# Kernel optimization log

Measured on AMD Instinct MI355X. Metric: run time of the kernel, lower is better.

The kernel has to match this reference:

```python
import jax, jax.numpy as jnp
import numpy as np

GAMMA = 0.5

def setup_inputs() -> dict:
    key = jax.random.key(0)
    k1, k2 = jax.random.split(key)
    x = jax.random.normal(k1, (4096, 256), dtype=jnp.float32)
    W = jax.random.normal(k2, (256, 512), dtype=jnp.float32)
    return {"x": x, "W": W}

def reference(x, W):
    # difference: (B, D, N) = (B, D, 1) - (D, N)
    diff = x[:, :, None] - W[None, :, :]
    sq_dist = jnp.sum(diff * diff, axis=1)          # (B, N)
    return jnp.exp(-GAMMA * sq_dist)                # (B, N)
```

## Files before the change

kernel.cpp:

```cpp
#include <hip/hip_runtime.h>


#define GAMMA 0.5f
#define B_  4096
#define D_  256
#define N_  512
#define BM  64
#define BN  64
#define LDT 264

typedef __attribute__((ext_vector_type(8))) short bf16x8;
typedef __attribute__((ext_vector_type(4))) float f32x4;
typedef __attribute__((ext_vector_type(4))) unsigned short u16x4;
typedef __attribute__((ext_vector_type(4))) float float4v;

__device__ __forceinline__ unsigned short f2bf(float f) {
    union { float f; unsigned int i; } u; u.f = f;
    return (unsigned short)(u.i >> 16);
}
__device__ __forceinline__ float bf2f(unsigned short h) {
    union { unsigned int i; float f; } u; u.i = ((unsigned int)h) << 16;
    return u.f;
}

__global__ __launch_bounds__(256, 4)
void rbf_kernel(const float* __restrict__ x, const float* __restrict__ W,
                float* __restrict__ out) {
    __shared__ unsigned short xs[BM][LDT];
    __shared__ float x2s[BM];

    const int tid = threadIdx.x;

    const int bid = blockIdx.x;
    const int wgid = (bid & 7) * 64 + (bid >> 3);
    const int bx = wgid & 7;
    const int by = wgid >> 3;

    {
        const float4v* xg = (const float4v*)(x + (size_t)by * BM * D_);
        #pragma unroll
        for (int t = 0; t < 16; ++t) {
            int i = tid + t * 256;
            int r = i >> 6, c4 = i & 63;
            float4v v = xg[i];
            u16x4 p = { f2bf(v.x), f2bf(v.y), f2bf(v.z), f2bf(v.w) };
            *(u16x4*)&xs[r][c4 * 4] = p;
        }
    }
    __syncthreads();

    {
        int row = tid >> 2, q = tid & 3;
        float s = 0.f;
        #pragma unroll
        for (int c = 0; c < 8; ++c) {
            bf16x8 v = *(const bf16x8*)&xs[row][q * 64 + c * 8];
            #pragma unroll
            for (int j = 0; j < 8; ++j) { float f = bf2f((unsigned short)v[j]); s += f * f; }
        }
        s += __shfl_xor(s, 1);
        s += __shfl_xor(s, 2);
        if (q == 0) x2s[row] = s;
    }
    __syncthreads();

    const int l = tid & 63, w = tid >> 6;
    const int wr = w >> 1, wc = w & 1;
    const int lr = l & 15, g = l >> 4;

    const float* Wg = W + bx * BN + wc * 32 + lr;
    float w2p0 = 0.f, w2p1 = 0.f;
    f32x4 accs[2][2] = {{{0,0,0,0},{0,0,0,0}},{{0,0,0,0},{0,0,0,0}}};

    #pragma unroll
    for (int kk = 0; kk < 8; ++kk) {
        const int k0 = kk * 32 + g * 8;
        const float* wp = Wg + (size_t)k0 * N_;
        float w0[8], w1[8];
        #pragma unroll
        for (int j = 0; j < 8; ++j) {
            w0[j] = wp[(size_t)j * N_];
            w1[j] = wp[(size_t)j * N_ + 16];
        }
        bf16x8 b0, b1;
        #pragma unroll
        for (int j = 0; j < 8; ++j) {
            b0[j] = (short)f2bf(w0[j]); b1[j] = (short)f2bf(w1[j]);
            w2p0 += w0[j] * w0[j];      w2p1 += w1[j] * w1[j];
        }
        bf16x8 a0 = *(const bf16x8*)&xs[wr * 32 + lr][k0];
        bf16x8 a1 = *(const bf16x8*)&xs[wr * 32 + 16 + lr][k0];
        accs[0][0] = __builtin_amdgcn_mfma_f32_16x16x32_bf16(a0, b0, accs[0][0], 0, 0, 0);
        accs[0][1] = __builtin_amdgcn_mfma_f32_16x16x32_bf16(a0, b1, accs[0][1], 0, 0, 0);
        accs[1][0] = __builtin_amdgcn_mfma_f32_16x16x32_bf16(a1, b0, accs[1][0], 0, 0, 0);
        accs[1][1] = __builtin_amdgcn_mfma_f32_16x16x32_bf16(a1, b1, accs[1][1], 0, 0, 0);
    }

    w2p0 += __shfl_xor(w2p0, 16); w2p0 += __shfl_xor(w2p0, 32);
    w2p1 += __shfl_xor(w2p1, 16); w2p1 += __shfl_xor(w2p1, 32);

    const float c2l = -(GAMMA) * 1.4426950408889634f;
    float* outp = out + (size_t)(by * BM) * N_ + bx * BN;
    #pragma unroll
    for (int m = 0; m < 2; ++m) {
        #pragma unroll
        for (int n = 0; n < 2; ++n) {
            float w2v = n ? w2p1 : w2p0;
            int ac = wc * 32 + n * 16 + lr;
            #pragma unroll
            for (int i = 0; i < 4; ++i) {
                int ar = wr * 32 + m * 16 + g * 4 + i;
                float s = x2s[ar] + w2v - 2.f * accs[m][n][i];
                outp[(size_t)ar * N_ + ac] = exp2f(s * c2l);
            }
        }
    }
}

extern "C" void kernel_launch(void* const* d_in, const int* in_sizes, int n_in,
                              void* d_out, int out_size, void* d_ws, size_t ws_size,
                              hipStream_t stream) {
    const float* x = (const float*)d_in[0];
    const float* W = (const float*)d_in[1];
    float* out = (float*)d_out;
    rbf_kernel<<<dim3(512), dim3(256), 0, stream>>>(x, W, out);
}
```

Before: 61.79 us.

## Stage W tile in shared memory as transposed bf16 and compute norms from LDS

The W tile is now loaded cooperatively with coalesced float4 reads, transposed and converted to bf16 in LDS. Before, each lane issued strided scalar global loads across rows inside the MFMA loop. The W squared norms are now computed from the bf16 LDS copy in the same pass as the x norms, so W norms are taken from rounded values, slightly changing precision. LDS use roughly doubles and the launch bound's min-blocks hint drops to 2, which may reduce occupancy.

```diff
diff --git a/kernel.cpp b/kernel.cpp
--- a/kernel.cpp
+++ b/kernel.cpp
@@ -23,11 +23,13 @@
     return u.f;
 }
 
-__global__ __launch_bounds__(256, 4)
+__global__ __launch_bounds__(256, 2)
 void rbf_kernel(const float* __restrict__ x, const float* __restrict__ W,
                 float* __restrict__ out) {
     __shared__ unsigned short xs[BM][LDT];
+    __shared__ unsigned short ws[BN][LDT];
     __shared__ float x2s[BM];
+    __shared__ float w2s[BN];
 
     const int tid = threadIdx.x;
 
@@ -47,20 +49,44 @@
             *(u16x4*)&xs[r][c4 * 4] = p;
         }
     }
+
+    {
+        const float* Wg = W + bx * BN;
+        #pragma unroll
+        for (int t = 0; t < 4; ++t) {
+            int i = tid + t * 256;
+            int kb = i >> 4, nb = i & 15;
+            const float* p0 = Wg + (size_t)(kb * 4) * N_ + nb * 4;
+            float4v r0 = *(const float4v*)(p0);
+            float4v r1 = *(const float4v*)(p0 + N_);
+            float4v r2 = *(const float4v*)(p0 + 2 * N_);
+            float4v r3 = *(const float4v*)(p0 + 3 * N_);
+            u16x4 c0 = { f2bf(r0.x), f2bf(r1.x), f2bf(r2.x), f2bf(r3.x) };
+            u16x4 c1 = { f2bf(r0.y), f2bf(r1.y), f2bf(r2.y), f2bf(r3.y) };
+            u16x4 c2 = { f2bf(r0.z), f2bf(r1.z), f2bf(r2.z), f2bf(r3.z) };
+            u16x4 c3 = { f2bf(r0.w), f2bf(r1.w), f2bf(r2.w), f2bf(r3.w) };
+            *(u16x4*)&ws[nb * 4 + 0][kb * 4] = c0;
+            *(u16x4*)&ws[nb * 4 + 1][kb * 4] = c1;
+            *(u16x4*)&ws[nb * 4 + 2][kb * 4] = c2;
+            *(u16x4*)&ws[nb * 4 + 3][kb * 4] = c3;
+        }
+    }
     __syncthreads();
 
     {
-        int row = tid >> 2, q = tid & 3;
+        int row = tid >> 1, q = tid & 1;
+        const unsigned short* base = (row < BM) ? &xs[row][0] : &ws[row - BM][0];
         float s = 0.f;
         #pragma unroll
-        for (int c = 0; c < 8; ++c) {
-            bf16x8 v = *(const bf16x8*)&xs[row][q * 64 + c * 8];
+        for (int c = 0; c < 16; ++c) {
+            bf16x8 v = *(const bf16x8*)&base[q * 128 + c * 8];
             #pragma unroll
             for (int j = 0; j < 8; ++j) { float f = bf2f((unsigned short)v[j]); s += f * f; }
         }
         s += __shfl_xor(s, 1);
-        s += __shfl_xor(s, 2);
-        if (q == 0) x2s[row] = s;
+        if (q == 0) {
+            if (row < BM) x2s[row] = s; else w2s[row - BM] = s;
+        }
     }
     __syncthreads();
 
@@ -68,36 +94,19 @@
     const int wr = w >> 1, wc = w & 1;
     const int lr = l & 15, g = l >> 4;
 
-    const float* Wg = W + bx * BN + wc * 32 + lr;
-    float w2p0 = 0.f, w2p1 = 0.f;
     f32x4 accs[2][2] = {{{0,0,0,0},{0,0,0,0}},{{0,0,0,0},{0,0,0,0}}};
-
     #pragma unroll
     for (int kk = 0; kk < 8; ++kk) {
         const int k0 = kk * 32 + g * 8;
-        const float* wp = Wg + (size_t)k0 * N_;
-        float w0[8], w1[8];
-        #pragma unroll
-        for (int j = 0; j < 8; ++j) {
-            w0[j] = wp[(size_t)j * N_];
-            w1[j] = wp[(size_t)j * N_ + 16];
-        }
-        bf16x8 b0, b1;
-        #pragma unroll
-        for (int j = 0; j < 8; ++j) {
-            b0[j] = (short)f2bf(w0[j]); b1[j] = (short)f2bf(w1[j]);
-            w2p0 += w0[j] * w0[j];      w2p1 += w1[j] * w1[j];
-        }
         bf16x8 a0 = *(const bf16x8*)&xs[wr * 32 + lr][k0];
         bf16x8 a1 = *(const bf16x8*)&xs[wr * 32 + 16 + lr][k0];
+        bf16x8 b0 = *(const bf16x8*)&ws[wc * 32 + lr][k0];
+        bf16x8 b1 = *(const bf16x8*)&ws[wc * 32 + 16 + lr][k0];
         accs[0][0] = __builtin_amdgcn_mfma_f32_16x16x32_bf16(a0, b0, accs[0][0], 0, 0, 0);
         accs[0][1] = __builtin_amdgcn_mfma_f32_16x16x32_bf16(a0, b1, accs[0][1], 0, 0, 0);
         accs[1][0] = __builtin_amdgcn_mfma_f32_16x16x32_bf16(a1, b0, accs[1][0], 0, 0, 0);
         accs[1][1] = __builtin_amdgcn_mfma_f32_16x16x32_bf16(a1, b1, accs[1][1], 0, 0, 0);
     }
-
-    w2p0 += __shfl_xor(w2p0, 16); w2p0 += __shfl_xor(w2p0, 32);
-    w2p1 += __shfl_xor(w2p1, 16); w2p1 += __shfl_xor(w2p1, 32);
 
     const float c2l = -(GAMMA) * 1.4426950408889634f;
     float* outp = out + (size_t)(by * BM) * N_ + bx * BN;
@@ -105,8 +114,8 @@
     for (int m = 0; m < 2; ++m) {
         #pragma unroll
         for (int n = 0; n < 2; ++n) {
-            float w2v = n ? w2p1 : w2p0;
             int ac = wc * 32 + n * 16 + lr;
+            float w2v = w2s[ac];
             #pragma unroll
             for (int i = 0; i < 4; ++i) {
                 int ar = wr * 32 + m * 16 + g * 4 + i;
```

New measurement: 62.97 us. Within noise of the previous version (+1.9%).

## Split bf16 conversion and norms into a prep kernel, feed MFMA from global

Applied to the files above, without the earlier changes.

Adds a prep kernel that converts x to bf16, transposes W into a bf16 N-major layout, and computes the row norms of x and W once. The main kernel then loads MFMA operands directly from these precomputed buffers instead of staging x in LDS and re-reading and converting strided fp32 W in every block. This removes redundant per-block W conversion and the LDS and barrier phase. In exchange it adds a second launch and workspace traffic, and the x norms are now computed from fp32 rather than bf16-rounded values.

```diff
diff --git a/kernel.cpp b/kernel.cpp
--- a/kernel.cpp
+++ b/kernel.cpp
@@ -5,112 +5,103 @@
 #define B_  4096
 #define D_  256
 #define N_  512
-#define BM  64
-#define BN  64
-#define LDT 264
 
 typedef __attribute__((ext_vector_type(8))) short bf16x8;
 typedef __attribute__((ext_vector_type(4))) float f32x4;
-typedef __attribute__((ext_vector_type(4))) unsigned short u16x4;
 typedef __attribute__((ext_vector_type(4))) float float4v;
 
 __device__ __forceinline__ unsigned short f2bf(float f) {
     union { float f; unsigned int i; } u; u.f = f;
     return (unsigned short)(u.i >> 16);
 }
-__device__ __forceinline__ float bf2f(unsigned short h) {
-    union { unsigned int i; float f; } u; u.i = ((unsigned int)h) << 16;
-    return u.f;
+
+__global__ __launch_bounds__(256)
+void rbf_prep(const float* __restrict__ x, const float* __restrict__ W,
+              unsigned short* __restrict__ xbf, unsigned short* __restrict__ wt,
+              float* __restrict__ x2, float* __restrict__ w2) {
+    const int bid = blockIdx.x, tid = threadIdx.x;
+    const int q = tid & 3;
+    if (bid < 64) {
+        const int row = bid * 64 + (tid >> 2);
+        const float* xp = x + (size_t)row * D_ + q * 64;
+        unsigned short* op = xbf + (size_t)row * D_ + q * 64;
+        float s = 0.f;
+        #pragma unroll
+        for (int c = 0; c < 8; ++c) {
+            float4v v0 = *(const float4v*)(xp + c * 8);
+            float4v v1 = *(const float4v*)(xp + c * 8 + 4);
+            s += v0.x*v0.x + v0.y*v0.y + v0.z*v0.z + v0.w*v0.w;
+            s += v1.x*v1.x + v1.y*v1.y + v1.z*v1.z + v1.w*v1.w;
+            bf16x8 o = { (short)f2bf(v0.x), (short)f2bf(v0.y), (short)f2bf(v0.z), (short)f2bf(v0.w),
+                         (short)f2bf(v1.x), (short)f2bf(v1.y), (short)f2bf(v1.z), (short)f2bf(v1.w) };
+            *(bf16x8*)(op + c * 8) = o;
+        }
+        s += __shfl_xor(s, 1); s += __shfl_xor(s, 2);
+        if (q == 0) x2[row] = s;
+    } else {
+        const int n = (bid - 64) * 64 + (tid >> 2);
+        const float* wp = W + (size_t)(q * 64) * N_ + n;
+        unsigned short* op = wt + (size_t)n * D_ + q * 64;
+        float s = 0.f;
+        #pragma unroll
+        for (int c = 0; c < 8; ++c) {
+            bf16x8 o;
+            #pragma unroll
+            for (int j = 0; j < 8; ++j) {
+                float f = wp[(size_t)(c * 8 + j) * N_];
+                s += f * f;
+                o[j] = (short)f2bf(f);
+            }
+            *(bf16x8*)(op + c * 8) = o;
+        }
+        s += __shfl_xor(s, 1); s += __shfl_xor(s, 2);
+        if (q == 0) w2[n] = s;
+    }
 }
 
-__global__ __launch_bounds__(256, 4)
-void rbf_kernel(const float* __restrict__ x, const float* __restrict__ W,
-                float* __restrict__ out) {
-    __shared__ unsigned short xs[BM][LDT];
-    __shared__ float x2s[BM];
-
-    const int tid = threadIdx.x;
-
-    const int bid = blockIdx.x;
+__global__ __launch_bounds__(256, 2)
+void rbf_main(const unsigned short* __restrict__ xbf, const unsigned short* __restrict__ wt,
+              const float* __restrict__ x2, const float* __restrict__ w2,
+              float* __restrict__ out) {
+    const int tid = threadIdx.x, bid = blockIdx.x;
     const int wgid = (bid & 7) * 64 + (bid >> 3);
     const int bx = wgid & 7;
     const int by = wgid >> 3;
-
-    {
-        const float4v* xg = (const float4v*)(x + (size_t)by * BM * D_);
-        #pragma unroll
-        for (int t = 0; t < 16; ++t) {
-            int i = tid + t * 256;
-            int r = i >> 6, c4 = i & 63;
-            float4v v = xg[i];
-            u16x4 p = { f2bf(v.x), f2bf(v.y), f2bf(v.z), f2bf(v.w) };
-            *(u16x4*)&xs[r][c4 * 4] = p;
-        }
-    }
-    __syncthreads();
-
-    {
-        int row = tid >> 2, q = tid & 3;
-        float s = 0.f;
-        #pragma unroll
-        for (int c = 0; c < 8; ++c) {
-            bf16x8 v = *(const bf16x8*)&xs[row][q * 64 + c * 8];
-            #pragma unroll
-            for (int j = 0; j < 8; ++j) { float f = bf2f((unsigned short)v[j]); s += f * f; }
-        }
-        s += __shfl_xor(s, 1);
-        s += __shfl_xor(s, 2);
-        if (q == 0) x2s[row] = s;
-    }
-    __syncthreads();
 
     const int l = tid & 63, w = tid >> 6;
     const int wr = w >> 1, wc = w & 1;
     const int lr = l & 15, g = l >> 4;
 
-    const float* Wg = W + bx * BN + wc * 32 + lr;
-    float w2p0 = 0.f, w2p1 = 0.f;
-    f32x4 accs[2][2] = {{{0,0,0,0},{0,0,0,0}},{{0,0,0,0},{0,0,0,0}}};
+    const unsigned short* ap0 = xbf + (size_t)(by * 64 + wr * 32 + lr) * D_ + g * 8;
+    const unsigned short* ap1 = ap0 + 16 * D_;
+    const unsigned short* bp0 = wt + (size_t)(bx * 64 + wc * 32 + lr) * D_ + g * 8;
+    const unsigned short* bp1 = bp0 + 16 * D_;
 
+    f32x4 acc[2][2] = {{{0,0,0,0},{0,0,0,0}},{{0,0,0,0},{0,0,0,0}}};
     #pragma unroll
     for (int kk = 0; kk < 8; ++kk) {
-        const int k0 = kk * 32 + g * 8;
-        const float* wp = Wg + (size_t)k0 * N_;
-        float w0[8], w1[8];
-        #pragma unroll
-        for (int j = 0; j < 8; ++j) {
-            w0[j] = wp[(size_t)j * N_];
-            w1[j] = wp[(size_t)j * N_ + 16];
-        }
-        bf16x8 b0, b1;
-        #pragma unroll
-        for (int j = 0; j < 8; ++j) {
-            b0[j] = (short)f2bf(w0[j]); b1[j] = (short)f2bf(w1[j]);
-            w2p0 += w0[j] * w0[j];      w2p1 += w1[j] * w1[j];
-        }
-        bf16x8 a0 = *(const bf16x8*)&xs[wr * 32 + lr][k0];
-        bf16x8 a1 = *(const bf16x8*)&xs[wr * 32 + 16 + lr][k0];
-        accs[0][0] = __builtin_amdgcn_mfma_f32_16x16x32_bf16(a0, b0, accs[0][0], 0, 0, 0);
-        accs[0][1] = __builtin_amdgcn_mfma_f32_16x16x32_bf16(a0, b1, accs[0][1], 0, 0, 0);
-        accs[1][0] = __builtin_amdgcn_mfma_f32_16x16x32_bf16(a1, b0, accs[1][0], 0, 0, 0);
-        accs[1][1] = __builtin_amdgcn_mfma_f32_16x16x32_bf16(a1, b1, accs[1][1], 0, 0, 0);
+        bf16x8 a0 = *(const bf16x8*)(ap0 + kk * 32);
+        bf16x8 a1 = *(const bf16x8*)(ap1 + kk * 32);
+        bf16x8 b0 = *(const bf16x8*)(bp0 + kk * 32);
+        bf16x8 b1 = *(const bf16x8*)(bp1 + kk * 32);
+        acc[0][0] = __builtin_amdgcn_mfma_f32_16x16x32_bf16(a0, b0, acc[0][0], 0, 0, 0);
+        acc[0][1] = __builtin_amdgcn_mfma_f32_16x16x32_bf16(a0, b1, acc[0][1], 0, 0, 0);
+        acc[1][0] = __builtin_amdgcn_mfma_f32_16x16x32_bf16(a1, b0, acc[1][0], 0, 0, 0);
+        acc[1][1] = __builtin_amdgcn_mfma_f32_16x16x32_bf16(a1, b1, acc[1][1], 0, 0, 0);
     }
 
-    w2p0 += __shfl_xor(w2p0, 16); w2p0 += __shfl_xor(w2p0, 32);
-    w2p1 += __shfl_xor(w2p1, 16); w2p1 += __shfl_xor(w2p1, 32);
-
     const float c2l = -(GAMMA) * 1.4426950408889634f;
-    float* outp = out + (size_t)(by * BM) * N_ + bx * BN;
+    float* outp = out + (size_t)(by * 64) * N_ + bx * 64;
     #pragma unroll
     for (int m = 0; m < 2; ++m) {
         #pragma unroll
         for (int n = 0; n < 2; ++n) {
-            float w2v = n ? w2p1 : w2p0;
-            int ac = wc * 32 + n * 16 + lr;
+            const int ac = wc * 32 + n * 16 + lr;
+            const float w2v = w2[bx * 64 + ac];
             #pragma unroll
             for (int i = 0; i < 4; ++i) {
-                int ar = wr * 32 + m * 16 + g * 4 + i;
-                float s = x2s[ar] + w2v - 2.f * accs[m][n][i];
+                const int ar = wr * 32 + m * 16 + g * 4 + i;
+                const float s = x2[by * 64 + ar] + w2v - 2.f * acc[m][n][i];
                 outp[(size_t)ar * N_ + ac] = exp2f(s * c2l);
             }
         }
@@ -123,5 +114,13 @@
     const float* x = (const float*)d_in[0];
     const float* W = (const float*)d_in[1];
     float* out = (float*)d_out;
-    rbf_kernel<<<dim3(512), dim3(256), 0, stream>>>(x, W, out);
+
+    char* ws = (char*)d_ws;
+    unsigned short* xbf = (unsigned short*)(ws);
+    unsigned short* wt  = (unsigned short*)(ws + (2u << 20));
+    float* x2 = (float*)(ws + (3u << 20));
+    float* w2 = (float*)(ws + (3u << 20) + (64u << 10));
+
+    rbf_prep<<<dim3(72), dim3(256), 0, stream>>>(x, W, xbf, wt, x2, w2);
+    rbf_main<<<dim3(512), dim3(256), 0, stream>>>(xbf, wt, x2, w2, out);
 }
```

Result: slower. 70.06 us (+13.4%).
